# Optimization experiments

Hardware: AMD Instinct MI355X
Metric: run time of the kernel (lower is better)

The kernel has to match this reference:

```python
import jax, jax.numpy as jnp
import numpy as np

N = 50000
IN_FEAT = 128
HIDDEN = 128
NUM_CLASS = 64
E = 1600000


def setup_inputs() -> dict:
    key = jax.random.key(0)
    ks = jax.random.split(key, 10)
    s = 1.0 / np.sqrt(HIDDEN)
    return {
        "x": jax.random.normal(ks[0], (N, IN_FEAT), dtype=jnp.float32),
        "edge_index": jax.random.randint(ks[1], (2, E), 0, N, dtype=jnp.int64),
        "We": jax.random.uniform(ks[2], (IN_FEAT, HIDDEN), jnp.float32, -s, s),
        "be": jax.random.uniform(ks[3], (HIDDEN,), jnp.float32, -s, s),
        "W1": jax.random.uniform(ks[4], (HIDDEN, HIDDEN), jnp.float32, -s, s),
        "b1": jax.random.uniform(ks[5], (HIDDEN,), jnp.float32, -s, s),
        "W2": jax.random.uniform(ks[6], (HIDDEN, HIDDEN), jnp.float32, -s, s),
        "b2": jax.random.uniform(ks[7], (HIDDEN,), jnp.float32, -s, s),
        "Wo": jax.random.uniform(ks[8], (HIDDEN, NUM_CLASS), jnp.float32, -s, s),
        "bo": jax.random.uniform(ks[9], (NUM_CLASS,), jnp.float32, -s, s),
    }


def _gcn_conv(h, src, dst, norm, W, b, n):
    # h: [N, H]; src/dst/norm: [E+N] (self-loops appended); GCNConv math:
    # out = scatter_add(norm * (h @ W)[src] -> dst) + b
    h = h @ W
    msg = h[src] * norm[:, None]  # gather + scale  [E+N, H]
    out = jax.ops.segment_sum(msg, dst, num_segments=n)
    return out + b


def reference(x, edge_index, We, be, W1, b1, W2, b2, Wo, bo):
    n = x.shape[0]
    loops = jnp.arange(n, dtype=edge_index.dtype)
    src = jnp.concatenate([edge_index[0], loops])
    dst = jnp.concatenate([edge_index[1], loops])
    # symmetric normalization D^{-1/2} (A+I) D^{-1/2}
    deg = jax.ops.segment_sum(jnp.ones_like(dst, dtype=x.dtype), dst, num_segments=n)
    dinv = jnp.where(deg > 0, jax.lax.rsqrt(deg), 0.0)
    norm = dinv[src] * dinv[dst]

    h = x @ We + be                       # encoder
    h = jax.nn.relu(_gcn_conv(h, src, dst, norm, W1, b1, n))
    h = jax.nn.relu(_gcn_conv(h, src, dst, norm, W2, b2, n))
    return h @ Wo + bo                    # decoder
```

## Files before the change

kernel.cpp:

```cpp
#include <hip/hip_runtime.h>
#include <hip/hip_fp16.h>


#define WS_ALIGN(x) (((x) + 255) & ~(size_t)255)
#define RS 100
#define EPT 16

typedef _Float16 f16x8 __attribute__((ext_vector_type(8)));
typedef float f32x4 __attribute__((ext_vector_type(4)));

__global__ void detect_i64_kernel(const unsigned* __restrict__ p, int* __restrict__ flag) {
    __shared__ int any;
    if (threadIdx.x == 0) any = 0;
    __syncthreads();
    int nz = 0;
    for (int i = threadIdx.x; i < 2048; i += blockDim.x)
        nz |= (p[2 * i + 1] != 0u) ? 1 : 0;
    if (nz) atomicOr(&any, 1);
    __syncthreads();
    if (threadIdx.x == 0) *flag = (any == 0) ? 1 : 0;
}

__global__ void zero_u32_kernel(unsigned* __restrict__ a, int n) {
    int i = blockIdx.x * blockDim.x + threadIdx.x;
    if (i < n) a[i] = 0u;
}

__global__ __launch_bounds__(256) void bucket_kernel(
    const void* __restrict__ ep, const int* __restrict__ flag,
    unsigned* __restrict__ bkt, unsigned* __restrict__ bfill_pad,
    int E, int nbuck, int capB) {
    __shared__ unsigned lcnt[1024];
    __shared__ unsigned gb[1024];
    const int tid = threadIdx.x;
    for (int i = tid; i < nbuck; i += 256) lcnt[i] = 0;
    __syncthreads();
    const int base = blockIdx.x * (256 * EPT);
    const int i64 = *flag;
    unsigned pk[EPT]; unsigned rk[EPT]; int pr[EPT];
#pragma unroll
    for (int k = 0; k < EPT; ++k) {
        int i = base + k * 256 + tid;
        pr[k] = -1;
        if (i < E) {
            int s, d;
            if (i64) {
                const long long* p = (const long long*)ep;
                s = (int)p[i]; d = (int)p[(size_t)E + i];
            } else {
                const int* p = (const int*)ep;
                s = p[i]; d = p[(size_t)E + i];
            }
            int part = d / RS;
            int ld = d - part * RS;
            pk[k] = ((unsigned)ld << 24) | (unsigned)s;
            pr[k] = part;
            rk[k] = atomicAdd(&lcnt[part], 1u);
        }
    }
    __syncthreads();
    for (int i = tid; i < nbuck; i += 256)
        gb[i] = atomicAdd(&bfill_pad[i << 4], lcnt[i]);
    __syncthreads();
#pragma unroll
    for (int k = 0; k < EPT; ++k) {
        if (pr[k] >= 0) {
            unsigned pos = gb[pr[k]] + rk[k];
            if (pos < (unsigned)capB)
                bkt[(size_t)pr[k] * capB + pos] = pk[k];
        }
    }
}

__global__ __launch_bounds__(512) void bucket_scan_kernel(
    const unsigned* __restrict__ bfill_pad, unsigned* __restrict__ ebase,
    int* __restrict__ rowp, int nbuck, int capB, int n) {
    __shared__ unsigned lds[512];
    const int tid = threadIdx.x;
    unsigned v = 0;
    if (tid < nbuck) {
        v = bfill_pad[tid << 4];
        if (v > (unsigned)capB) v = capB;
    }
    lds[tid] = v;
    __syncthreads();
    for (int off = 1; off < 512; off <<= 1) {
        unsigned add = (tid >= off) ? lds[tid - off] : 0;
        __syncthreads();
        lds[tid] += add;
        __syncthreads();
    }
    if (tid < nbuck) ebase[tid] = lds[tid] - v;
    if (tid == 511) rowp[n] = (int)lds[511];
}

__global__ __launch_bounds__(256) void csr_from_bucket_kernel(
    const unsigned* __restrict__ bkt, const unsigned* __restrict__ bfill_pad,
    const unsigned* __restrict__ ebase,
    int* __restrict__ rowp, float* __restrict__ dinv, int* __restrict__ col,
    int capB, int n) {
    __shared__ unsigned hist[RS];
    __shared__ int fillo[RS];
    const int p = blockIdx.x;
    const int tid = threadIdx.x;
    for (int i = tid; i < RS; i += 256) hist[i] = 0;
    __syncthreads();
    unsigned cnt = bfill_pad[p << 4];
    if (cnt > (unsigned)capB) cnt = capB;
    const unsigned* bp = bkt + (size_t)p * capB;
    for (unsigned e = tid; e < cnt; e += 256)
        atomicAdd(&hist[bp[e] >> 24], 1u);
    __syncthreads();
    if (tid == 0) {
        int run = (int)ebase[p];
        for (int i = 0; i < RS; ++i) { fillo[i] = run; run += (int)hist[i]; }
    }
    __syncthreads();
    const int lo = p * RS;
    for (int i = tid; i < RS; i += 256) {
        int node = lo + i;
        if (node < n) {
            rowp[node] = fillo[i];
            dinv[node] = rsqrtf((float)(hist[i] + 1u));
        }
    }
    for (unsigned e = tid; e < cnt; e += 256) {
        unsigned u = bp[e];
        int ld = (int)(u >> 24);
        int pos = atomicAdd(&fillo[ld], 1);
        col[pos] = (int)(u & 0xFFFFFFu);
    }
}

__global__ __launch_bounds__(256) void agg_pull_kernel(
    const int* __restrict__ rowp, const int* __restrict__ col,
    const float* __restrict__ dinv, const __half* __restrict__ t,
    const float* __restrict__ bias, __half* __restrict__ out, int n) {
    int node = blockIdx.x * 8 + (threadIdx.x >> 5);
    int lane = threadIdx.x & 31;
    if (node >= n) return;
    const uint2* T = (const uint2*)t;
    int j0 = rowp[node], j1 = rowp[node + 1];
    float dn = dinv[node];

#define H4_TO_F(raw, fa, fb)                                   \
    float2 fa = __half22float2(*(const __half2*)&raw.x);       \
    float2 fb = __half22float2(*(const __half2*)&raw.y);

    uint2 sraw = T[(size_t)node * 32 + lane];
    H4_TO_F(sraw, s01, s23)
    float4 acc;
    acc.x = s01.x * dn; acc.y = s01.y * dn; acc.z = s23.x * dn; acc.w = s23.y * dn;

    int j = j0;
    for (; j + 3 < j1; j += 4) {
        int c0 = col[j], c1 = col[j + 1], c2 = col[j + 2], c3 = col[j + 3];
        float w0 = dinv[c0], w1 = dinv[c1], w2 = dinv[c2], w3 = dinv[c3];
        uint2 r0 = T[(size_t)c0 * 32 + lane];
        uint2 r1 = T[(size_t)c1 * 32 + lane];
        uint2 r2 = T[(size_t)c2 * 32 + lane];
        uint2 r3 = T[(size_t)c3 * 32 + lane];
        H4_TO_F(r0, a01, a23)
        H4_TO_F(r1, b01, b23)
        H4_TO_F(r2, c01, c23)
        H4_TO_F(r3, d01, d23)
        acc.x = fmaf(a01.x, w0, acc.x); acc.y = fmaf(a01.y, w0, acc.y);
        acc.z = fmaf(a23.x, w0, acc.z); acc.w = fmaf(a23.y, w0, acc.w);
        acc.x = fmaf(b01.x, w1, acc.x); acc.y = fmaf(b01.y, w1, acc.y);
        acc.z = fmaf(b23.x, w1, acc.z); acc.w = fmaf(b23.y, w1, acc.w);
        acc.x = fmaf(c01.x, w2, acc.x); acc.y = fmaf(c01.y, w2, acc.y);
        acc.z = fmaf(c23.x, w2, acc.z); acc.w = fmaf(c23.y, w2, acc.w);
        acc.x = fmaf(d01.x, w3, acc.x); acc.y = fmaf(d01.y, w3, acc.y);
        acc.z = fmaf(d23.x, w3, acc.z); acc.w = fmaf(d23.y, w3, acc.w);
    }
    for (; j < j1; ++j) {
        int c = col[j];
        float w = dinv[c];
        uint2 raw = T[(size_t)c * 32 + lane];
        H4_TO_F(raw, f01, f23)
        acc.x = fmaf(f01.x, w, acc.x); acc.y = fmaf(f01.y, w, acc.y);
        acc.z = fmaf(f23.x, w, acc.z); acc.w = fmaf(f23.y, w, acc.w);
    }
#undef H4_TO_F
    float4 b = ((const float4*)bias)[lane];
    float ox = fmaxf(fmaf(acc.x, dn, b.x), 0.f);
    float oy = fmaxf(fmaf(acc.y, dn, b.y), 0.f);
    float oz = fmaxf(fmaf(acc.z, dn, b.z), 0.f);
    float ow = fmaxf(fmaf(acc.w, dn, b.w), 0.f);
    __half2 h01 = __floats2half2_rn(ox, oy);
    __half2 h23 = __floats2half2_rn(oz, ow);
    uint2 packed;
    packed.x = *(unsigned*)&h01;
    packed.y = *(unsigned*)&h23;
    ((uint2*)(out + (size_t)node * 128))[lane] = packed;
}

__global__ void f32_to_f16_kernel(const float* __restrict__ in, __half* __restrict__ out, int n8) {
    int i = blockIdx.x * blockDim.x + threadIdx.x;
    if (i >= n8) return;
    const float4* in4 = (const float4*)in;
    float4 v0 = in4[2 * i], v1 = in4[2 * i + 1];
    __half2 h0 = __floats2half2_rn(v0.x, v0.y);
    __half2 h1 = __floats2half2_rn(v0.z, v0.w);
    __half2 h2 = __floats2half2_rn(v1.x, v1.y);
    __half2 h3 = __floats2half2_rn(v1.z, v1.w);
    uint4 p;
    p.x = *(unsigned*)&h0; p.y = *(unsigned*)&h1;
    p.z = *(unsigned*)&h2; p.w = *(unsigned*)&h3;
    *(uint4*)(out + (size_t)i * 8) = p;
}

__global__ void wfrag_kernel(const float* __restrict__ W, __half* __restrict__ Wf, int ncol) {
    int t = blockIdx.x * blockDim.x + threadIdx.x;
    int total = (ncol >> 4) * 4 * 64;
    if (t >= total) return;
    int lane = t & 63;
    int ks = (t >> 6) & 3;
    int c0 = t >> 8;
    int colw = c0 * 16 + (lane & 15);
    int k0 = ks * 32 + ((lane >> 4) << 3);
    __half vals[8];
#pragma unroll
    for (int j = 0; j < 8; ++j) vals[j] = __float2half(W[(size_t)(k0 + j) * ncol + colw]);
    *(uint4*)(Wf + (size_t)t * 8) = *(uint4*)vals;
}

__global__ __launch_bounds__(256) void gemm_mfma_kernel(
    const __half* __restrict__ A, const __half* __restrict__ Wf,
    const float* __restrict__ bias, void* __restrict__ C,
    int n, int ncol, int c_fp32) {
    const int wave = threadIdx.x >> 6;
    const int lane = threadIdx.x & 63;
    const int row0 = blockIdx.x * 64 + wave * 16;
    int ar = row0 + (lane & 15);
    if (ar >= n) ar = n - 1;
    const __half* abase = A + (size_t)ar * 128 + ((lane >> 4) << 3);
    f16x8 a0 = *(const f16x8*)(abase);
    f16x8 a1 = *(const f16x8*)(abase + 32);
    f16x8 a2 = *(const f16x8*)(abase + 64);
    f16x8 a3 = *(const f16x8*)(abase + 96);
    const int ncc = ncol >> 4;
    const int cic = lane & 15;
    const int rbase = (lane >> 4) << 2;
    for (int c0 = 0; c0 < ncc; ++c0) {
        const f16x8* wf = (const f16x8*)Wf + (size_t)c0 * 256 + lane;
        f32x4 acc = {0.f, 0.f, 0.f, 0.f};
        acc = __builtin_amdgcn_mfma_f32_16x16x32_f16(a0, wf[0],   acc, 0, 0, 0);
        acc = __builtin_amdgcn_mfma_f32_16x16x32_f16(a1, wf[64],  acc, 0, 0, 0);
        acc = __builtin_amdgcn_mfma_f32_16x16x32_f16(a2, wf[128], acc, 0, 0, 0);
        acc = __builtin_amdgcn_mfma_f32_16x16x32_f16(a3, wf[192], acc, 0, 0, 0);
        int colc = (c0 << 4) + cic;
        float bv = bias ? bias[colc] : 0.f;
#pragma unroll
        for (int r = 0; r < 4; ++r) {
            int row = row0 + rbase + r;
            if (row < n) {
                float v = acc[r] + bv;
                if (c_fp32) ((float*)C)[(size_t)row * ncol + colc] = v;
                else        ((__half*)C)[(size_t)row * ncol + colc] = __float2half(v);
            }
        }
    }
}

extern "C" void kernel_launch(void* const* d_in, const int* in_sizes, int n_in,
                              void* d_out, int out_size, void* d_ws, size_t ws_size,
                              hipStream_t stream) {
    const float* x  = (const float*)d_in[0];
    const void*  ei = d_in[1];
    const float* We = (const float*)d_in[2];
    const float* be = (const float*)d_in[3];
    const float* W1 = (const float*)d_in[4];
    const float* b1 = (const float*)d_in[5];
    const float* W2 = (const float*)d_in[6];
    const float* b2 = (const float*)d_in[7];
    const float* Wo = (const float*)d_in[8];
    const float* bo = (const float*)d_in[9];
    const int N = in_sizes[0] / 128;
    const int E = in_sizes[1] / 2;
    const int NC = in_sizes[9];
    const int nbuck = (N + RS - 1) / RS;
    const int capB = (E + nbuck - 1) / nbuck + 512;

    char* ws = (char*)d_ws;
    size_t off = 0;
    int*      flag = (int*)(ws + off);      off += 256;
    unsigned* bfil = (unsigned*)(ws + off); off += WS_ALIGN((size_t)nbuck * 64);
    unsigned* ebas = (unsigned*)(ws + off); off += WS_ALIGN((size_t)nbuck * 4);
    unsigned* bkt  = (unsigned*)(ws + off); off += WS_ALIGN((size_t)nbuck * capB * 4);
    float*    dinv = (float*)(ws + off);    off += WS_ALIGN((size_t)N * 4);
    int*      rowp = (int*)(ws + off);      off += WS_ALIGN((size_t)(N + 1) * 4);
    int*      colw = (int*)(ws + off);      off += WS_ALIGN((size_t)E * 4);
    __half*   WeF  = (__half*)(ws + off);   off += WS_ALIGN((size_t)128 * 128 * 2);
    __half*   W1F  = (__half*)(ws + off);   off += WS_ALIGN((size_t)128 * 128 * 2);
    __half*   W2F  = (__half*)(ws + off);   off += WS_ALIGN((size_t)128 * 128 * 2);
    __half*   WoF  = (__half*)(ws + off);   off += WS_ALIGN((size_t)128 * 64 * 2);
    __half*   xH   = (__half*)(ws + off);   off += WS_ALIGN((size_t)N * 128 * 2);
    __half*   hA   = (__half*)(ws + off);   off += WS_ALIGN((size_t)N * 128 * 2);
    __half*   tH   = (__half*)(ws + off);   off += WS_ALIGN((size_t)N * 128 * 2);

    const int nb_bucket = (E + 256 * EPT - 1) / (256 * EPT);
    const int nb_zero = (nbuck * 16 + 255) / 256;
    dim3 blk(256);

    detect_i64_kernel<<<1, 256, 0, stream>>>((const unsigned*)ei, flag);
    zero_u32_kernel<<<nb_zero, blk, 0, stream>>>(bfil, nbuck * 16);
    bucket_kernel<<<nb_bucket, blk, 0, stream>>>(ei, flag, bkt, bfil, E, nbuck, capB);
    bucket_scan_kernel<<<1, 512, 0, stream>>>(bfil, ebas, rowp, nbuck, capB, N);
    csr_from_bucket_kernel<<<nbuck, blk, 0, stream>>>(bkt, bfil, ebas, rowp, dinv, colw, capB, N);

    wfrag_kernel<<<8, 256, 0, stream>>>(We, WeF, 128);
    wfrag_kernel<<<8, 256, 0, stream>>>(W1, W1F, 128);
    wfrag_kernel<<<8, 256, 0, stream>>>(W2, W2F, 128);
    wfrag_kernel<<<4, 256, 0, stream>>>(Wo, WoF, NC);
    f32_to_f16_kernel<<<(N * 16 + 255) / 256, 256, 0, stream>>>(x, xH, N * 16);

    const int gemm_blocks = (N + 63) / 64;
    const int agg_blocks = (N + 7) / 8;

    gemm_mfma_kernel<<<gemm_blocks, blk, 0, stream>>>(xH, WeF, be, hA, N, 128, 0);
    gemm_mfma_kernel<<<gemm_blocks, blk, 0, stream>>>(hA, W1F, nullptr, tH, N, 128, 0);
    agg_pull_kernel<<<agg_blocks, blk, 0, stream>>>(rowp, colw, dinv, tH, b1, hA, N);
    gemm_mfma_kernel<<<gemm_blocks, blk, 0, stream>>>(hA, W2F, nullptr, tH, N, 128, 0);
    agg_pull_kernel<<<agg_blocks, blk, 0, stream>>>(rowp, colw, dinv, tH, b2, hA, N);
    gemm_mfma_kernel<<<gemm_blocks, blk, 0, stream>>>(hA, WoF, bo, d_out, N, NC, 1);
}
```

Baseline: 227.2 us.

## Fold source-degree scaling into GEMM epilogue and rework edge bucketing

Result: slower. 238.1 us (+4.8%).

```diff
diff --git a/kernel.cpp b/kernel.cpp
--- a/kernel.cpp
+++ b/kernel.cpp
@@ -4,7 +4,7 @@
 
 #define WS_ALIGN(x) (((x) + 255) & ~(size_t)255)
 #define RS 100
-#define EPT 16
+#define BCHUNK 8192
 
 typedef _Float16 f16x8 __attribute__((ext_vector_type(8)));
 typedef float f32x4 __attribute__((ext_vector_type(4)));
@@ -30,44 +30,52 @@
     const void* __restrict__ ep, const int* __restrict__ flag,
     unsigned* __restrict__ bkt, unsigned* __restrict__ bfill_pad,
     int E, int nbuck, int capB) {
-    __shared__ unsigned lcnt[1024];
-    __shared__ unsigned gb[1024];
+    __shared__ unsigned lcnt[512];
+    __shared__ unsigned gcur[512];
     const int tid = threadIdx.x;
     for (int i = tid; i < nbuck; i += 256) lcnt[i] = 0;
     __syncthreads();
-    const int base = blockIdx.x * (256 * EPT);
+    const int base = blockIdx.x * BCHUNK;
+    const int end = min(base + BCHUNK, E);
     const int i64 = *flag;
-    unsigned pk[EPT]; unsigned rk[EPT]; int pr[EPT];
-#pragma unroll
-    for (int k = 0; k < EPT; ++k) {
-        int i = base + k * 256 + tid;
-        pr[k] = -1;
-        if (i < E) {
-            int s, d;
-            if (i64) {
-                const long long* p = (const long long*)ep;
-                s = (int)p[i]; d = (int)p[(size_t)E + i];
-            } else {
-                const int* p = (const int*)ep;
-                s = p[i]; d = p[(size_t)E + i];
-            }
+    if (i64) {
+        const long long* p = (const long long*)ep;
+        for (int i = base + tid; i < end; i += 256) {
+            int d = (int)p[(size_t)E + i];
+            atomicAdd(&lcnt[d / RS], 1u);
+        }
+    } else {
+        const int* p = (const int*)ep;
+        for (int i = base + tid; i < end; i += 256) {
+            int d = p[(size_t)E + i];
+            atomicAdd(&lcnt[d / RS], 1u);
+        }
+    }
+    __syncthreads();
+    for (int i = tid; i < nbuck; i += 256)
+        gcur[i] = atomicAdd(&bfill_pad[i << 4], lcnt[i]);
+    __syncthreads();
+    if (i64) {
+        const long long* p = (const long long*)ep;
+        for (int i = base + tid; i < end; i += 256) {
+            int s = (int)p[i];
+            int d = (int)p[(size_t)E + i];
             int part = d / RS;
             int ld = d - part * RS;
-            pk[k] = ((unsigned)ld << 24) | (unsigned)s;
-            pr[k] = part;
-            rk[k] = atomicAdd(&lcnt[part], 1u);
-        }
-    }
-    __syncthreads();
-    for (int i = tid; i < nbuck; i += 256)
-        gb[i] = atomicAdd(&bfill_pad[i << 4], lcnt[i]);
-    __syncthreads();
-#pragma unroll
-    for (int k = 0; k < EPT; ++k) {
-        if (pr[k] >= 0) {
-            unsigned pos = gb[pr[k]] + rk[k];
+            unsigned pos = atomicAdd(&gcur[part], 1u);
             if (pos < (unsigned)capB)
-                bkt[(size_t)pr[k] * capB + pos] = pk[k];
+                bkt[(size_t)part * capB + pos] = ((unsigned)ld << 24) | (unsigned)s;
+        }
+    } else {
+        const int* p = (const int*)ep;
+        for (int i = base + tid; i < end; i += 256) {
+            int s = p[i];
+            int d = p[(size_t)E + i];
+            int part = d / RS;
+            int ld = d - part * RS;
+            unsigned pos = atomicAdd(&gcur[part], 1u);
+            if (pos < (unsigned)capB)
+                bkt[(size_t)part * capB + pos] = ((unsigned)ld << 24) | (unsigned)s;
         }
     }
 }
@@ -143,45 +151,48 @@
     int j0 = rowp[node], j1 = rowp[node + 1];
     float dn = dinv[node];
 
-#define H4_TO_F(raw, fa, fb)                                   \
-    float2 fa = __half22float2(*(const __half2*)&raw.x);       \
-    float2 fb = __half22float2(*(const __half2*)&raw.y);
-
     uint2 sraw = T[(size_t)node * 32 + lane];
-    H4_TO_F(sraw, s01, s23)
-    float4 acc;
-    acc.x = s01.x * dn; acc.y = s01.y * dn; acc.z = s23.x * dn; acc.w = s23.y * dn;
+    float2 s01 = __half22float2(*(const __half2*)&sraw.x);
+    float2 s23 = __half22float2(*(const __half2*)&sraw.y);
+    float4 acc = make_float4(s01.x, s01.y, s23.x, s23.y);
 
     int j = j0;
+    for (; j + 7 < j1; j += 8) {
+        int c[8];
+        uint2 r[8];
+#pragma unroll
+        for (int k = 0; k < 8; ++k) c[k] = __builtin_nontemporal_load(col + j + k);
+#pragma unroll
+        for (int k = 0; k < 8; ++k) r[k] = T[(size_t)c[k] * 32 + lane];
+#pragma unroll
+        for (int k = 0; k < 8; ++k) {
+            float2 f01 = __half22float2(*(const __half2*)&r[k].x);
+            float2 f23 = __half22float2(*(const __half2*)&r[k].y);
+            acc.x += f01.x; acc.y += f01.y; acc.z += f23.x; acc.w += f23.y;
+        }
+    }
     for (; j + 3 < j1; j += 4) {
-        int c0 = col[j], c1 = col[j + 1], c2 = col[j + 2], c3 = col[j + 3];
-        float w0 = dinv[c0], w1 = dinv[c1], w2 = dinv[c2], w3 = dinv[c3];
-        uint2 r0 = T[(size_t)c0 * 32 + lane];
-        uint2 r1 = T[(size_t)c1 * 32 + lane];
-        uint2 r2 = T[(size_t)c2 * 32 + lane];
-        uint2 r3 = T[(size_t)c3 * 32 + lane];
-        H4_TO_F(r0, a01, a23)
-        H4_TO_F(r1, b01, b23)
-        H4_TO_F(r2, c01, c23)
-        H4_TO_F(r3, d01, d23)
-        acc.x = fmaf(a01.x, w0, acc.x); acc.y = fmaf(a01.y, w0, acc.y);
-        acc.z = fmaf(a23.x, w0, acc.z); acc.w = fmaf(a23.y, w0, acc.w);
-        acc.x = fmaf(b01.x, w1, acc.x); acc.y = fmaf(b01.y, w1, acc.y);
-        acc.z = fmaf(b23.x, w1, acc.z); acc.w = fmaf(b23.y, w1, acc.w);
-        acc.x = fmaf(c01.x, w2, acc.x); acc.y = fmaf(c01.y, w2, acc.y);
-        acc.z = fmaf(c23.x, w2, acc.z); acc.w = fmaf(c23.y, w2, acc.w);
-        acc.x = fmaf(d01.x, w3, acc.x); acc.y = fmaf(d01.y, w3, acc.y);
-        acc.z = fmaf(d23.x, w3, acc.z); acc.w = fmaf(d23.y, w3, acc.w);
+        int c[4];
+        uint2 r[4];
+#pragma unroll
+        for (int k = 0; k < 4; ++k) c[k] = __builtin_nontemporal_load(col + j + k);
+#pragma unroll
+        for (int k = 0; k < 4; ++k) r[k] = T[(size_t)c[k] * 32 + lane];
+#pragma unroll
+        for (int k = 0; k < 4; ++k) {
+            float2 f01 = __half22float2(*(const __half2*)&r[k].x);
+            float2 f23 = __half22float2(*(const __half2*)&r[k].y);
+            acc.x += f01.x; acc.y += f01.y; acc.z += f23.x; acc.w += f23.y;
+        }
     }
     for (; j < j1; ++j) {
-        int c = col[j];
-        float w = dinv[c];
+        int c = __builtin_nontemporal_load(col + j);
         uint2 raw = T[(size_t)c * 32 + lane];
-        H4_TO_F(raw, f01, f23)
-        acc.x = fmaf(f01.x, w, acc.x); acc.y = fmaf(f01.y, w, acc.y);
-        acc.z = fmaf(f23.x, w, acc.z); acc.w = fmaf(f23.y, w, acc.w);
-    }
-#undef H4_TO_F
+        float2 f01 = __half22float2(*(const __half2*)&raw.x);
+        float2 f23 = __half22float2(*(const __half2*)&raw.y);
+        acc.x += f01.x; acc.y += f01.y; acc.z += f23.x; acc.w += f23.y;
+    }
+
     float4 b = ((const float4*)bias)[lane];
     float ox = fmaxf(fmaf(acc.x, dn, b.x), 0.f);
     float oy = fmaxf(fmaf(acc.y, dn, b.y), 0.f);
@@ -227,8 +238,8 @@
 
 __global__ __launch_bounds__(256) void gemm_mfma_kernel(
     const __half* __restrict__ A, const __half* __restrict__ Wf,
-    const float* __restrict__ bias, void* __restrict__ C,
-    int n, int ncol, int c_fp32) {
+    const float* __restrict__ bias, const float* __restrict__ rowscale,
+    void* __restrict__ C, int n, int ncol, int c_fp32) {
     const int wave = threadIdx.x >> 6;
     const int lane = threadIdx.x & 63;
     const int row0 = blockIdx.x * 64 + wave * 16;
@@ -242,6 +253,12 @@
     const int ncc = ncol >> 4;
     const int cic = lane & 15;
     const int rbase = (lane >> 4) << 2;
+    float rs[4];
+#pragma unroll
+    for (int r = 0; r < 4; ++r) {
+        int row = row0 + rbase + r;
+        rs[r] = (rowscale && row < n) ? rowscale[row] : 1.f;
+    }
     for (int c0 = 0; c0 < ncc; ++c0) {
         const f16x8* wf = (const f16x8*)Wf + (size_t)c0 * 256 + lane;
         f32x4 acc = {0.f, 0.f, 0.f, 0.f};
@@ -255,7 +272,7 @@
         for (int r = 0; r < 4; ++r) {
             int row = row0 + rbase + r;
             if (row < n) {
-                float v = acc[r] + bv;
+                float v = acc[r] * rs[r] + bv;
                 if (c_fp32) ((float*)C)[(size_t)row * ncol + colc] = v;
                 else        ((__half*)C)[(size_t)row * ncol + colc] = __float2half(v);
             }
@@ -299,7 +316,7 @@
     __half*   hA   = (__half*)(ws + off);   off += WS_ALIGN((size_t)N * 128 * 2);
     __half*   tH   = (__half*)(ws + off);   off += WS_ALIGN((size_t)N * 128 * 2);
 
-    const int nb_bucket = (E + 256 * EPT - 1) / (256 * EPT);
+    const int nb_bucket = (E + BCHUNK - 1) / BCHUNK;
     const int nb_zero = (nbuck * 16 + 255) / 256;
     dim3 blk(256);
 
@@ -318,10 +335,10 @@
     const int gemm_blocks = (N + 63) / 64;
     const int agg_blocks = (N + 7) / 8;
 
-    gemm_mfma_kernel<<<gemm_blocks, blk, 0, stream>>>(xH, WeF, be, hA, N, 128, 0);
-    gemm_mfma_kernel<<<gemm_blocks, blk, 0, stream>>>(hA, W1F, nullptr, tH, N, 128, 0);
+    gemm_mfma_kernel<<<gemm_blocks, blk, 0, stream>>>(xH, WeF, be, nullptr, hA, N, 128, 0);
+    gemm_mfma_kernel<<<gemm_blocks, blk, 0, stream>>>(hA, W1F, nullptr, dinv, tH, N, 128, 0);
     agg_pull_kernel<<<agg_blocks, blk, 0, stream>>>(rowp, colw, dinv, tH, b1, hA, N);
-    gemm_mfma_kernel<<<gemm_blocks, blk, 0, stream>>>(hA, W2F, nullptr, tH, N, 128, 0);
+    gemm_mfma_kernel<<<gemm_blocks, blk, 0, stream>>>(hA, W2F, nullptr, dinv, tH, N, 128, 0);
     agg_pull_kernel<<<agg_blocks, blk, 0, stream>>>(rowp, colw, dinv, tH, b2, hA, N);
-    gemm_mfma_kernel<<<gemm_blocks, blk, 0, stream>>>(hA, WoF, bo, d_out, N, NC, 1);
-}
+    gemm_mfma_kernel<<<gemm_blocks, blk, 0, stream>>>(hA, WoF, bo, nullptr, d_out, N, NC, 1);
+}
```
